# Kernel tuning notes

Measured on AMD Instinct MI355X. Metric: run time of the kernel, lower is better.

Reference implementation:

```python
import jax, jax.numpy as jnp
import numpy as np

NEG_INF = -9e15  # matches -9000000000000000.0 in torch code
ALPHA = 0.2      # LeakyReLU negative slope


def setup_inputs() -> dict:
    key = jax.random.key(0)
    k1, k2, k3, k4 = jax.random.split(key, 4)
    B, N, Fin, Fout = 8, 2048, 256, 256
    h = jax.random.normal(k1, (B, N, Fin), dtype=jnp.float32)
    adj = jax.random.randint(k2, (B, N, N), 0, 2, dtype=jnp.int32)
    W = jax.random.normal(k3, (Fin, Fout), dtype=jnp.float32) * 0.05
    a = jax.random.normal(k4, (2 * Fout, 1), dtype=jnp.float32) * 0.05
    return {"h": h, "adj": adj, "W": W, "a": a}


def reference(h, adj, W, a):
    # h: [B,N,Fin], adj: [B,N,N], W: [Fin,Fout], a: [2*Fout,1]
    Fout = W.shape[1]
    Wh = jnp.matmul(h, W)                       # [B,N,Fout]
    # Decompose concat-based additive score: e_ij = LReLU(a1.Wh_i + a2.Wh_j)
    a1 = a[:Fout, 0]                            # source-node part
    a2 = a[Fout:, 0]                            # target-node part
    s1 = jnp.einsum('bnf,f->bn', Wh, a1)        # [B,N]
    s2 = jnp.einsum('bnf,f->bn', Wh, a2)        # [B,N]
    e = jax.nn.leaky_relu(s1[:, :, None] + s2[:, None, :], negative_slope=ALPHA)  # [B,N,N]
    attn = jnp.where(adj > 0, e, NEG_INF)
    attn = jax.nn.softmax(attn, axis=2)          # masked softmax over neighbors
    # dropout omitted (deterministic eval-mode reference)
    h_prime = jnp.matmul(attn, Wh)               # [B,N,Fout]
    return h_prime
```

## Files before the change

kernel.cpp:

```cpp
#include <hip/hip_runtime.h>
#include <cstdint>

#define ALPHA 0.2f

constexpr int NB = 8;
constexpr int NN = 2048;
constexpr int NF = 256;

typedef __attribute__((ext_vector_type(8))) short bf16x8;
typedef __attribute__((ext_vector_type(4))) float f32x4;

__device__ __forceinline__ float bf2f(unsigned short u) {
    union { unsigned int i; float f; } v;
    v.i = ((unsigned int)u) << 16;
    return v.f;
}
__device__ __forceinline__ unsigned short f2bf(float f) {
    union { float f; unsigned int i; } v;
    v.f = f;
    v.i += 0x7fffu + ((v.i >> 16) & 1);
    return (unsigned short)(v.i >> 16);
}

__global__ __launch_bounds__(256) void k_wt(const float* __restrict__ W,
                                            unsigned short* __restrict__ WT,
                                            float* __restrict__ s1,
                                            float* __restrict__ s2) {
    const int t = threadIdx.x;
    const int gid = blockIdx.x * 256 + t;
    s1[gid] = 0.f;
    s2[gid] = 0.f;
    const int k = blockIdx.x * 4 + (t >> 6);
    const int f0 = (t & 63) * 4;
    const float4 w = *(const float4*)&W[k * NF + f0];
    WT[(f0 + 0) * NF + k] = f2bf(w.x);
    WT[(f0 + 1) * NF + k] = f2bf(w.y);
    WT[(f0 + 2) * NF + k] = f2bf(w.z);
    WT[(f0 + 3) * NF + k] = f2bf(w.w);
}

__global__ __launch_bounds__(256, 4) void k_wh(const float* __restrict__ h,
                                               const unsigned short* __restrict__ WT,
                                               const float* __restrict__ a,
                                               unsigned short* __restrict__ WhT,
                                               float* __restrict__ s1,
                                               float* __restrict__ s2) {
    __shared__ __align__(16) unsigned short As[64][72];
    __shared__ __align__(16) unsigned short Bs[64][72];
    const int tid = threadIdx.x;
    const int lane = tid & 63;
    const int l16 = lane & 15;
    const int quad = lane >> 4;
    const int wave = tid >> 6;
    const int row0 = (blockIdx.x >> 2) * 64;
    const int col0 = (blockIdx.x & 3) * 64;
    const int bb = row0 >> 11;
    const int n0 = row0 & (NN - 1);
    const int mb = (wave & 1) * 32;
    const int nb = (wave >> 1) * 32;

    f32x4 acc[2][2];
#pragma unroll
    for (int mf = 0; mf < 2; ++mf)
#pragma unroll
        for (int nf = 0; nf < 2; ++nf) acc[mf][nf] = (f32x4){0.f, 0.f, 0.f, 0.f};

    for (int k0 = 0; k0 < NF; k0 += 64) {
#pragma unroll
        for (int it = 0; it < 4; ++it) {
            const int q = tid + it * 256;
            const int r = q >> 4;
            const int k4 = (q & 15) * 4;
            const float4 v = *(const float4*)&h[(size_t)(row0 + r) * NF + k0 + k4];
            ushort4 o;
            o.x = f2bf(v.x); o.y = f2bf(v.y); o.z = f2bf(v.z); o.w = f2bf(v.w);
            *(ushort4*)&As[r][k4] = o;
        }
#pragma unroll
        for (int it = 0; it < 2; ++it) {
            const int q = tid + it * 256;
            const int f = q >> 3;
            const int k8 = (q & 7) * 8;
            *(uint4*)&Bs[f][k8] =
                *(const uint4*)&WT[(size_t)(col0 + f) * NF + k0 + k8];
        }
        __syncthreads();
#pragma unroll
        for (int ks = 0; ks < 64; ks += 32) {
            bf16x8 av[2], bv[2];
#pragma unroll
            for (int mf = 0; mf < 2; ++mf)
                av[mf] = *(const bf16x8*)&As[mb + mf * 16 + l16][ks + quad * 8];
#pragma unroll
            for (int nf = 0; nf < 2; ++nf)
                bv[nf] = *(const bf16x8*)&Bs[nb + nf * 16 + l16][ks + quad * 8];
#pragma unroll
            for (int mf = 0; mf < 2; ++mf)
#pragma unroll
                for (int nf = 0; nf < 2; ++nf)
                    acc[mf][nf] = __builtin_amdgcn_mfma_f32_16x16x32_bf16(
                        av[mf], bv[nf], acc[mf][nf], 0, 0, 0);
        }
        __syncthreads();
    }

#pragma unroll
    for (int mf = 0; mf < 2; ++mf) {
#pragma unroll
        for (int nf = 0; nf < 2; ++nf) {
            const size_t f = col0 + nb + nf * 16 + l16;
            const int nr = n0 + mb + mf * 16 + quad * 4;
            ushort4 o;
            o.x = f2bf(acc[mf][nf][0]);
            o.y = f2bf(acc[mf][nf][1]);
            o.z = f2bf(acc[mf][nf][2]);
            o.w = f2bf(acc[mf][nf][3]);
            *(ushort4*)&WhT[((size_t)bb * NF + f) * NN + nr] = o;
        }
    }

    float a1v[2], a2v[2];
#pragma unroll
    for (int nf = 0; nf < 2; ++nf) {
        const int f = col0 + nb + nf * 16 + l16;
        a1v[nf] = a[f];
        a2v[nf] = a[NF + f];
    }
#pragma unroll
    for (int mf = 0; mf < 2; ++mf) {
#pragma unroll
        for (int r = 0; r < 4; ++r) {
            float p1 = acc[mf][0][r] * a1v[0] + acc[mf][1][r] * a1v[1];
            float p2 = acc[mf][0][r] * a2v[0] + acc[mf][1][r] * a2v[1];
            p1 += __shfl_xor(p1, 1); p2 += __shfl_xor(p2, 1);
            p1 += __shfl_xor(p1, 2); p2 += __shfl_xor(p2, 2);
            p1 += __shfl_xor(p1, 4); p2 += __shfl_xor(p2, 4);
            p1 += __shfl_xor(p1, 8); p2 += __shfl_xor(p2, 8);
            if (l16 == 0) {
                const int n = n0 + mb + mf * 16 + quad * 4 + r;
                atomicAdd(&s1[bb * NN + n], p1);
                atomicAdd(&s2[bb * NN + n], p2);
            }
        }
    }
}

__global__ __launch_bounds__(256, 3) void k_attn(const unsigned short* __restrict__ WhT,
                                                 const int* __restrict__ adj,
                                                 const float* __restrict__ s1g,
                                                 const float* __restrict__ s2g,
                                                 float* __restrict__ out) {
    __shared__ __align__(16) unsigned short WhsT[256][72];
    __shared__ __align__(16) unsigned short Pb[32][72];
    __shared__ float s1_s[32];
    __shared__ float l_s[32];

    const int tid = threadIdx.x;
    const int lane = tid & 63;
    const int l16 = lane & 15;
    const int quad = lane >> 4;
    const int wave = tid >> 6;
    const int bb = blockIdx.x >> 6;
    const int i0 = (blockIdx.x & 63) * 32;

    if (tid < 32) {
        s1_s[tid] = s1g[bb * NN + i0 + tid];
        l_s[tid] = 0.f;
    }
    __syncthreads();

    f32x4 acc[2][4];
#pragma unroll
    for (int m = 0; m < 2; ++m)
#pragma unroll
        for (int nf = 0; nf < 4; ++nf) acc[m][nf] = (f32x4){0.f, 0.f, 0.f, 0.f};

    const size_t whtBase = (size_t)bb * NF * NN;
    const size_t adjBase = (size_t)bb * NN * NN;
    const float* s2b = s2g + bb * NN;

    const int whF = tid >> 3;
    const int whK = (tid & 7) * 8;
    const int pIr = tid >> 4;
    const int pKq = (tid & 15) * 4;

    const unsigned short* whP = &WhT[whtBase + (size_t)whF * NN + whK];
    const int* adjP0 = &adj[adjBase + (size_t)(i0 + pIr) * NN + pKq];
    const int* adjP1 = adjP0 + 16 * NN;
    const float* s2P = &s2b[pKq];

    uint4 w0, w1, w2, w3, w4, w5, w6, w7;
    int4 am0, am1;
    float4 sv0, sv1;

#define LOAD_TILE(J0)                                                         \
    do {                                                                      \
        const int j0_ = (J0);                                                 \
        w0 = *(const uint4*)&whP[(size_t)(0 * 32) * NN + j0_];                \
        w1 = *(const uint4*)&whP[(size_t)(1 * 32) * NN + j0_];                \
        w2 = *(const uint4*)&whP[(size_t)(2 * 32) * NN + j0_];                \
        w3 = *(const uint4*)&whP[(size_t)(3 * 32) * NN + j0_];                \
        w4 = *(const uint4*)&whP[(size_t)(4 * 32) * NN + j0_];                \
        w5 = *(const uint4*)&whP[(size_t)(5 * 32) * NN + j0_];                \
        w6 = *(const uint4*)&whP[(size_t)(6 * 32) * NN + j0_];                \
        w7 = *(const uint4*)&whP[(size_t)(7 * 32) * NN + j0_];                \
        am0 = *(const int4*)&adjP0[j0_];                                      \
        am1 = *(const int4*)&adjP1[j0_];                                      \
        sv0 = *(const float4*)&s2P[j0_];                                      \
        sv1 = sv0;                                                            \
    } while (0)

    LOAD_TILE(0);

    for (int t = 0; t < NN / 64; ++t) {
        *(uint4*)&WhsT[whF + 0 * 32][whK] = w0;
        *(uint4*)&WhsT[whF + 1 * 32][whK] = w1;
        *(uint4*)&WhsT[whF + 2 * 32][whK] = w2;
        *(uint4*)&WhsT[whF + 3 * 32][whK] = w3;
        *(uint4*)&WhsT[whF + 4 * 32][whK] = w4;
        *(uint4*)&WhsT[whF + 5 * 32][whK] = w5;
        *(uint4*)&WhsT[whF + 6 * 32][whK] = w6;
        *(uint4*)&WhsT[whF + 7 * 32][whK] = w7;
#pragma unroll
        for (int it = 0; it < 2; ++it) {
            const int ir = pIr + it * 16;
            const int4 av = it ? am1 : am0;
            const float4 s2v = it ? sv1 : sv0;
            const float s1v = s1_s[ir];
            float x0 = s1v + s2v.x, x1 = s1v + s2v.y;
            float x2 = s1v + s2v.z, x3 = s1v + s2v.w;
            x0 = x0 > 0.f ? x0 : ALPHA * x0;
            x1 = x1 > 0.f ? x1 : ALPHA * x1;
            x2 = x2 > 0.f ? x2 : ALPHA * x2;
            x3 = x3 > 0.f ? x3 : ALPHA * x3;
            const float p0 = av.x > 0 ? __expf(x0) : 0.f;
            const float p1 = av.y > 0 ? __expf(x1) : 0.f;
            const float p2 = av.z > 0 ? __expf(x2) : 0.f;
            const float p3 = av.w > 0 ? __expf(x3) : 0.f;
            uint2 pk;
            pk.x = (unsigned int)f2bf(p0) | ((unsigned int)f2bf(p1) << 16);
            pk.y = (unsigned int)f2bf(p2) | ((unsigned int)f2bf(p3) << 16);
            *(uint2*)&Pb[ir][pKq] = pk;
            float ps = (p0 + p1) + (p2 + p3);
            ps += __shfl_xor(ps, 8);
            ps += __shfl_xor(ps, 4);
            ps += __shfl_xor(ps, 2);
            ps += __shfl_xor(ps, 1);
            if ((tid & 15) == 0) l_s[ir] += ps;
        }
        __syncthreads();
        if (t + 1 < NN / 64) LOAD_TILE((t + 1) * 64);
        const int f0 = wave * 64;
#pragma unroll
        for (int k0 = 0; k0 < 64; k0 += 32) {
            bf16x8 af[2];
#pragma unroll
            for (int m = 0; m < 2; ++m)
                af[m] = *(const bf16x8*)&Pb[m * 16 + l16][k0 + quad * 8];
#pragma unroll
            for (int nf = 0; nf < 4; ++nf) {
                const bf16x8 bfr =
                    *(const bf16x8*)&WhsT[f0 + nf * 16 + l16][k0 + quad * 8];
#pragma unroll
                for (int m = 0; m < 2; ++m)
                    acc[m][nf] = __builtin_amdgcn_mfma_f32_16x16x32_bf16(
                        af[m], bfr, acc[m][nf], 0, 0, 0);
            }
        }
        __syncthreads();
    }
#undef LOAD_TILE

    if (tid < 32) l_s[tid] = 1.0f / l_s[tid];
    __syncthreads();

    const int f0 = wave * 64;
#pragma unroll
    for (int m = 0; m < 2; ++m) {
#pragma unroll
        for (int r = 0; r < 4; ++r) {
            const int row = m * 16 + quad * 4 + r;
            const float inv = l_s[row];
#pragma unroll
            for (int nf = 0; nf < 4; ++nf) {
                out[((size_t)bb * NN + i0 + row) * NF + f0 + nf * 16 + l16] =
                    acc[m][nf][r] * inv;
            }
        }
    }
}

extern "C" void kernel_launch(void* const* d_in, const int* in_sizes, int n_in,
                              void* d_out, int out_size, void* d_ws, size_t ws_size,
                              hipStream_t stream) {
    const float* h = (const float*)d_in[0];
    const int* adj = (const int*)d_in[1];
    const float* W = (const float*)d_in[2];
    const float* a = (const float*)d_in[3];
    float* out = (float*)d_out;

    unsigned short* WhT = (unsigned short*)d_ws;
    float* s1 = (float*)((char*)d_ws + (size_t)NB * NN * NF * sizeof(unsigned short));
    float* s2 = s1 + (size_t)NB * NN;
    unsigned short* WT = (unsigned short*)(s2 + (size_t)NB * NN);

    k_wt<<<dim3(64), dim3(256), 0, stream>>>(W, WT, s1, s2);
    k_wh<<<dim3((NB * NN / 64) * (NF / 64)), dim3(256), 0, stream>>>(h, WT, a, WhT, s1, s2);
    k_attn<<<dim3(NB * (NN / 32)), dim3(256), 0, stream>>>(WhT, adj, s1, s2, out);
}
```

Baseline: 239.5 us.

## Prefetch next k-tile into registers in Wh GEMM and remap blocks across XCDs

```diff
diff --git a/kernel.cpp b/kernel.cpp
--- a/kernel.cpp
+++ b/kernel.cpp
@@ -52,8 +52,14 @@
     const int l16 = lane & 15;
     const int quad = lane >> 4;
     const int wave = tid >> 6;
-    const int row0 = (blockIdx.x >> 2) * 64;
-    const int col0 = (blockIdx.x & 3) * 64;
+
+    const int p = blockIdx.x;
+    const int xcd = p & 7;
+    const int q = p >> 3;
+    const int rowTile = xcd + (q >> 2) * 8;
+    const int row0 = rowTile * 64;
+    const int col0 = (q & 3) * 64;
+
     const int bb = row0 >> 11;
     const int n0 = row0 & (NN - 1);
     const int mb = (wave & 1) * 32;
@@ -65,26 +71,43 @@
 #pragma unroll
         for (int nf = 0; nf < 2; ++nf) acc[mf][nf] = (f32x4){0.f, 0.f, 0.f, 0.f};
 
+    const int r0 = tid >> 4;
+    const int k4 = (tid & 15) * 4;
+    const int f0w = tid >> 3;
+    const int k8 = (tid & 7) * 8;
+
+    const float* hP = &h[(size_t)(row0 + r0) * NF + k4];
+    const unsigned short* wP = &WT[(size_t)(col0 + f0w) * NF + k8];
+
+    float4 h0, h1, h2, h3;
+    uint4 wv0, wv1;
+
+#define LOADW(K0)                                                      \
+    do {                                                               \
+        h0 = *(const float4*)&hP[(size_t)(0 * 16) * NF + (K0)];        \
+        h1 = *(const float4*)&hP[(size_t)(1 * 16) * NF + (K0)];        \
+        h2 = *(const float4*)&hP[(size_t)(2 * 16) * NF + (K0)];        \
+        h3 = *(const float4*)&hP[(size_t)(3 * 16) * NF + (K0)];        \
+        wv0 = *(const uint4*)&wP[(K0)];                                \
+        wv1 = *(const uint4*)&wP[(size_t)32 * NF + (K0)];              \
+    } while (0)
+
+    LOADW(0);
+
     for (int k0 = 0; k0 < NF; k0 += 64) {
-#pragma unroll
-        for (int it = 0; it < 4; ++it) {
-            const int q = tid + it * 256;
-            const int r = q >> 4;
-            const int k4 = (q & 15) * 4;
-            const float4 v = *(const float4*)&h[(size_t)(row0 + r) * NF + k0 + k4];
-            ushort4 o;
-            o.x = f2bf(v.x); o.y = f2bf(v.y); o.z = f2bf(v.z); o.w = f2bf(v.w);
-            *(ushort4*)&As[r][k4] = o;
-        }
-#pragma unroll
-        for (int it = 0; it < 2; ++it) {
-            const int q = tid + it * 256;
-            const int f = q >> 3;
-            const int k8 = (q & 7) * 8;
-            *(uint4*)&Bs[f][k8] =
-                *(const uint4*)&WT[(size_t)(col0 + f) * NF + k0 + k8];
-        }
+        ushort4 o;
+        o.x = f2bf(h0.x); o.y = f2bf(h0.y); o.z = f2bf(h0.z); o.w = f2bf(h0.w);
+        *(ushort4*)&As[r0 + 0][k4] = o;
+        o.x = f2bf(h1.x); o.y = f2bf(h1.y); o.z = f2bf(h1.z); o.w = f2bf(h1.w);
+        *(ushort4*)&As[r0 + 16][k4] = o;
+        o.x = f2bf(h2.x); o.y = f2bf(h2.y); o.z = f2bf(h2.z); o.w = f2bf(h2.w);
+        *(ushort4*)&As[r0 + 32][k4] = o;
+        o.x = f2bf(h3.x); o.y = f2bf(h3.y); o.z = f2bf(h3.z); o.w = f2bf(h3.w);
+        *(ushort4*)&As[r0 + 48][k4] = o;
+        *(uint4*)&Bs[f0w][k8] = wv0;
+        *(uint4*)&Bs[f0w + 32][k8] = wv1;
         __syncthreads();
+        if (k0 + 64 < NF) LOADW(k0 + 64);
 #pragma unroll
         for (int ks = 0; ks < 64; ks += 32) {
             bf16x8 av[2], bv[2];
@@ -103,6 +126,7 @@
         }
         __syncthreads();
     }
+#undef LOADW
 
 #pragma unroll
     for (int mf = 0; mf < 2; ++mf) {
@@ -160,8 +184,8 @@
     const int l16 = lane & 15;
     const int quad = lane >> 4;
     const int wave = tid >> 6;
-    const int bb = blockIdx.x >> 6;
-    const int i0 = (blockIdx.x & 63) * 32;
+    const int bb = blockIdx.x & 7;
+    const int i0 = (blockIdx.x >> 3) * 32;
 
     if (tid < 32) {
         s1_s[tid] = s1g[bb * NN + i0 + tid];
```

Result: no change. 238.9 us (-0.3%).
